# Performance work log

Hardware: AMD Instinct MI355X
Metric: run time of the kernel (lower is better)

Reference implementation:

```python
import jax, jax.numpy as jnp
import numpy as np

N, E, IN, HID, OUT, H, G = 50000, 800000, 128, 32, 32, 4, 64
NEG_SLOPE = 0.2


def setup_inputs() -> dict:
    key = jax.random.key(0)
    ks = jax.random.split(key, 12)
    p = lambda k, s: jax.random.normal(k, s, jnp.float32) * 0.1
    x = jax.random.normal(ks[0], (N, IN), jnp.float32)
    edge_index = jax.random.randint(ks[1], (2, E), 0, N, dtype=jnp.int64)
    batch = jnp.sort(jax.random.randint(ks[2], (N,), 0, G, dtype=jnp.int64))
    return {
        'x': x, 'edge_index': edge_index, 'batch': batch,
        'W1': p(ks[3], (IN, H * HID)),
        'att_src1': p(ks[4], (H, HID)), 'att_dst1': p(ks[5], (H, HID)),
        'b1': jnp.zeros((H * HID,), jnp.float32),
        'W2': p(ks[6], (H * HID, H * OUT)),
        'att_src2': p(ks[7], (H, OUT)), 'att_dst2': p(ks[8], (H, OUT)),
        'b2': jnp.zeros((H * OUT,), jnp.float32),
        'lin_w': p(ks[9], (H * OUT, 1)),
        'lin_b': jnp.zeros((1,), jnp.float32),
    }


def gat_conv(x, src, dst, W, a_src, a_dst, b, heads, ch):
    # x: [N, F_in]; src/dst: [E'] with self-loops already appended.
    n = x.shape[0]
    h = (x @ W).reshape(n, heads, ch)                      # [N, H, C]
    alpha_s = jnp.einsum('nhc,hc->nh', h, a_src)           # [N, H]
    alpha_d = jnp.einsum('nhc,hc->nh', h, a_dst)
    e = jax.nn.leaky_relu(alpha_s[src] + alpha_d[dst], NEG_SLOPE)  # [E', H]
    # segment softmax over destination neighborhoods
    m = jax.ops.segment_max(e, dst, num_segments=n)
    m = jnp.where(jnp.isfinite(m), m, 0.0)
    ex = jnp.exp(e - m[dst])
    s = jax.ops.segment_sum(ex, dst, num_segments=n)
    alpha = ex / (s[dst] + 1e-16)                          # [E', H]
    out = jax.ops.segment_sum(alpha[:, :, None] * h[src], dst, num_segments=n)
    return out.reshape(n, heads * ch) + b


def reference(x, edge_index, batch, W1, att_src1, att_dst1, b1,
              W2, att_src2, att_dst2, b2, lin_w, lin_b):
    # add self-loops (PyG GATConv default add_self_loops=True)
    loops = jnp.arange(N, dtype=edge_index.dtype)
    src = jnp.concatenate([edge_index[0], loops])
    dst = jnp.concatenate([edge_index[1], loops])

    h = jax.nn.elu(gat_conv(x, src, dst, W1, att_src1, att_dst1, b1, H, HID))
    h = gat_conv(h, src, dst, W2, att_src2, att_dst2, b2, H, OUT)  # [N, H*OUT]

    # global mean + max pool per graph
    counts = jax.ops.segment_sum(jnp.ones((N,), h.dtype), batch, num_segments=G)
    mean_p = jax.ops.segment_sum(h, batch, num_segments=G) / jnp.maximum(counts, 1.0)[:, None]
    max_p = jax.ops.segment_max(h, batch, num_segments=G)
    max_p = jnp.where(jnp.isfinite(max_p), max_p, 0.0)
    pooled = mean_p + max_p                                # [G, H*OUT]
    return pooled @ lin_w + lin_b                          # [G, 1]
```

## Files before the change

kernel.cpp:

```cpp
#include <hip/hip_runtime.h>
#include <hip/hip_bf16.h>
#include <hip/hip_fp16.h>
#include <math.h>

#define NEG_SLOPE 0.2f
#define BCAP 64
#define LAYER_W 18432

typedef _Float16 half8 __attribute__((ext_vector_type(8)));
typedef _Float16 half4v __attribute__((ext_vector_type(4)));
typedef float f32x4 __attribute__((ext_vector_type(4)));


__device__ __forceinline__ int lbound(const int* __restrict__ a, int n, int key) {
    int lo = 0, hi = n;
    while (lo < hi) {
        int mid = (lo + hi) >> 1;
        if (a[mid] < key) lo = mid + 1; else hi = mid;
    }
    return lo;
}

__device__ __forceinline__ unsigned encf(float f) {
    unsigned u = __float_as_uint(f);
    return (u & 0x80000000u) ? ~u : (u | 0x80000000u);
}
__device__ __forceinline__ float decf(unsigned u) {
    return (u & 0x80000000u) ? __uint_as_float(u & 0x7FFFFFFFu) : __uint_as_float(~u);
}


__global__ void prep_kernel(const float* __restrict__ W1, const float* __restrict__ W2,
                            const float* __restrict__ as1, const float* __restrict__ ad1,
                            const float* __restrict__ as2, const float* __restrict__ ad2,
                            _Float16* __restrict__ wt_hi, _Float16* __restrict__ wt_lo,
                            int* __restrict__ cnt, float* __restrict__ gsum,
                            unsigned* __restrict__ gmax, unsigned short* __restrict__ col,
                            int n, int gtot) {
    int b = blockIdx.x;
    if (b < 72) {
        int lane = threadIdx.x;
        if (lane >= 64) return;
        int layer = b / 36;
        int rem = b % 36;
        int nt = rem >> 2;
        int kc = rem & 3;
        const float* W  = layer ? W2 : W1;
        const float* As = layer ? as2 : as1;
        const float* Ad = layer ? ad2 : ad1;
        int nn = lane & 15, q = lane >> 4;
        size_t base = (size_t)layer * LAYER_W + (size_t)((nt * 4 + kc) * 64 + lane) * 8;
        #pragma unroll
        for (int j = 0; j < 8; ++j) {
            int k = kc * 32 + q * 8 + j;
            float w = 0.f;
            if (nt < 8) {
                w = W[(size_t)k * 128 + nt * 16 + nn];
            } else if (nn < 4) {
                for (int c = 0; c < 32; ++c) w += W[(size_t)k * 128 + nn * 32 + c] * As[nn * 32 + c];
            } else if (nn < 8) {
                int hh = nn - 4;
                for (int c = 0; c < 32; ++c) w += W[(size_t)k * 128 + hh * 32 + c] * Ad[hh * 32 + c];
            }
            _Float16 hi = (_Float16)w;
            wt_hi[base + j] = hi;
            wt_lo[base + j] = (_Float16)(w - (float)hi);
        }
        return;
    }
    int i = (b - 72) * 256 + threadIdx.x;
    if (i < n) cnt[i] = 0;
    if (i < gtot) { gsum[i] = 0.f; gmax[i] = 0u; }
    if (i < n * 8) ((uint4*)col)[i] = make_uint4(0u, 0u, 0u, 0u);
}


__global__ void build_kernel(const int* __restrict__ src, const int* __restrict__ dst,
                             int* __restrict__ cnt, unsigned short* __restrict__ col,
                             int E, int n) {
    int part = blockIdx.x & 7;
    int bb   = blockIdx.x >> 3;
    int nb   = gridDim.x >> 3;
    int psz  = (n + 7) >> 3;
    int lo   = part * psz;
    int total = E + n;
    for (int i = bb * 256 + threadIdx.x; i < total; i += nb * 256) {
        int d = (i < E) ? dst[i] : (i - E);
        if (d < lo || d >= lo + psz) continue;
        int slot = atomicAdd(&cnt[d], 1);
        if (slot < BCAP) {
            int s = (i < E) ? src[i] : d;
            col[(size_t)d * BCAP + slot] = (unsigned short)s;
        }
    }
}


template <bool A16>
__global__ __launch_bounds__(256) void gemm_attn_kernel(
        const void* __restrict__ Araw,
        const _Float16* __restrict__ wt_hi, const _Float16* __restrict__ wt_lo,
        _Float16* __restrict__ H16, float* __restrict__ as_, float* __restrict__ ad_,
        int M) {
    __shared__ _Float16 a_st[128][136];

    int tid = threadIdx.x;
    int m0 = blockIdx.x * 128;

    if (A16) {
        const _Float16* A = (const _Float16*)Araw;
        #pragma unroll
        for (int t = 0; t < 8; ++t) {
            int f = tid + t * 256;
            int r = f >> 4;
            int c8 = (f & 15) << 3;
            int gr = m0 + r; if (gr >= M) gr = M - 1;
            *(half8*)&a_st[r][c8] = *(const half8*)(A + (size_t)gr * 128 + c8);
        }
    } else {
        const float* A = (const float*)Araw;
        #pragma unroll
        for (int t = 0; t < 16; ++t) {
            int f = tid + t * 256;
            int r = f >> 5;
            int c4 = (f & 31) << 2;
            int gr = m0 + r; if (gr >= M) gr = M - 1;
            const float4 v = *(const float4*)(A + (size_t)gr * 128 + c4);
            half4v hi = { (_Float16)v.x, (_Float16)v.y, (_Float16)v.z, (_Float16)v.w };
            *(half4v*)&a_st[r][c4] = hi;
        }
    }
    __syncthreads();

    int w = tid >> 6;
    int lane = tid & 63;
    int cbase = lane & 15;
    int q = lane >> 4;
    int mrow0 = (w << 5) + cbase;
    int mrow1 = mrow0 + 16;

    f32x4 acc0[9], acc1[9];
    #pragma unroll
    for (int nt = 0; nt < 9; ++nt) {
        acc0[nt] = (f32x4){0.f, 0.f, 0.f, 0.f};
        acc1[nt] = (f32x4){0.f, 0.f, 0.f, 0.f};
    }

    #pragma unroll
    for (int kc = 0; kc < 4; ++kc) {
        half8 ah0 = *(half8*)&a_st[mrow0][kc * 32 + q * 8];
        half8 ah1 = *(half8*)&a_st[mrow1][kc * 32 + q * 8];
        #pragma unroll
        for (int nt = 0; nt < 9; ++nt) {
            const half8 bh = *(const half8*)(wt_hi + (size_t)((nt * 4 + kc) * 64 + lane) * 8);
            const half8 bl = *(const half8*)(wt_lo + (size_t)((nt * 4 + kc) * 64 + lane) * 8);
            acc0[nt] = __builtin_amdgcn_mfma_f32_16x16x32_f16(ah0, bh, acc0[nt], 0, 0, 0);
            acc0[nt] = __builtin_amdgcn_mfma_f32_16x16x32_f16(ah0, bl, acc0[nt], 0, 0, 0);
            acc1[nt] = __builtin_amdgcn_mfma_f32_16x16x32_f16(ah1, bh, acc1[nt], 0, 0, 0);
            acc1[nt] = __builtin_amdgcn_mfma_f32_16x16x32_f16(ah1, bl, acc1[nt], 0, 0, 0);
        }
    }

    #pragma unroll
    for (int nt = 0; nt < 8; ++nt) {
        int c = nt * 16 + cbase;
        #pragma unroll
        for (int i = 0; i < 4; ++i) {
            int gr0 = m0 + (w << 5) + (q << 2) + i;
            int gr1 = gr0 + 16;
            if (gr0 < M) H16[(size_t)gr0 * 128 + c] = (_Float16)acc0[nt][i];
            if (gr1 < M) H16[(size_t)gr1 * 128 + c] = (_Float16)acc1[nt][i];
        }
    }
    if (cbase < 8) {
        #pragma unroll
        for (int i = 0; i < 4; ++i) {
            int gr0 = m0 + (w << 5) + (q << 2) + i;
            int gr1 = gr0 + 16;
            if (gr0 < M) {
                if (cbase < 4) as_[(size_t)gr0 * 4 + cbase]     = acc0[8][i];
                else           ad_[(size_t)gr0 * 4 + cbase - 4] = acc0[8][i];
            }
            if (gr1 < M) {
                if (cbase < 4) as_[(size_t)gr1 * 4 + cbase]     = acc1[8][i];
                else           ad_[(size_t)gr1 * 4 + cbase - 4] = acc1[8][i];
            }
        }
    }
}


__global__ __launch_bounds__(256) void agg_kernel(
        const int* __restrict__ cnt, const unsigned short* __restrict__ col,
        const _Float16* __restrict__ h16, const float* __restrict__ as_,
        const float* __restrict__ ad_, const float* __restrict__ bias,
        _Float16* __restrict__ out16, int n, int elu) {
    __shared__ float s_w[4][4][64];

    int wvb  = threadIdx.x >> 6;
    int lane = threadIdx.x & 63;
    int wv   = blockIdx.x * 4 + wvb;
    int valid = (wv < n);
    if (!valid) wv = n - 1;

    const unsigned short* crow = col + (size_t)wv * BCAP;
    int q = lane >> 4;
    int r = lane & 15;
    int head = r >> 2;
    unsigned roff = (unsigned)r << 4;
    const char* hbyte = (const char*)h16;

    ushort4 cr0 = *(const ushort4*)(crow + 4 * q);
    ushort4 cr1 = *(const ushort4*)(crow + 16 + 4 * q);
    half8 ha0 = *(const half8*)(hbyte + (((unsigned)cr0.x << 8) | roff));
    half8 ha1 = *(const half8*)(hbyte + (((unsigned)cr0.y << 8) | roff));
    half8 ha2 = *(const half8*)(hbyte + (((unsigned)cr0.z << 8) | roff));
    half8 ha3 = *(const half8*)(hbyte + (((unsigned)cr0.w << 8) | roff));
    half8 hb0 = *(const half8*)(hbyte + (((unsigned)cr1.x << 8) | roff));
    half8 hb1 = *(const half8*)(hbyte + (((unsigned)cr1.y << 8) | roff));
    half8 hb2 = *(const half8*)(hbyte + (((unsigned)cr1.z << 8) | roff));
    half8 hb3 = *(const half8*)(hbyte + (((unsigned)cr1.w << 8) | roff));

    int deg = cnt[wv]; if (deg > BCAP) deg = BCAP;

    const float4 adv = *(const float4*)(ad_ + (size_t)wv * 4);
    float w0 = 0.f, w1 = 0.f, w2 = 0.f, w3 = 0.f;
    if (lane < deg) {
        int s = crow[lane];
        const float4 av = *(const float4*)(as_ + (size_t)s * 4);
        float e0 = av.x + adv.x, e1 = av.y + adv.y;
        float e2 = av.z + adv.z, e3 = av.w + adv.w;
        w0 = __expf(fmaxf(e0, NEG_SLOPE * e0));
        w1 = __expf(fmaxf(e1, NEG_SLOPE * e1));
        w2 = __expf(fmaxf(e2, NEG_SLOPE * e2));
        w3 = __expf(fmaxf(e3, NEG_SLOPE * e3));
    }
    s_w[wvb][0][lane] = w0;
    s_w[wvb][1][lane] = w1;
    s_w[wvb][2][lane] = w2;
    s_w[wvb][3][lane] = w3;
    asm volatile("s_waitcnt lgkmcnt(0)" ::: "memory");

    f32x4 wa = *(const f32x4*)&s_w[wvb][head][4 * q];
    f32x4 wb = *(const f32x4*)&s_w[wvb][head][16 + 4 * q];
    float lsum = (wa.x + wa.y + wa.z + wa.w) + (wb.x + wb.y + wb.z + wb.w);
    float acc[8];
    #pragma unroll
    for (int j = 0; j < 8; ++j)
        acc[j] = wa.x * (float)ha0[j] + wa.y * (float)ha1[j]
               + wa.z * (float)ha2[j] + wa.w * (float)ha3[j]
               + wb.x * (float)hb0[j] + wb.y * (float)hb1[j]
               + wb.z * (float)hb2[j] + wb.w * (float)hb3[j];

    if (__builtin_expect(deg > 32, 0)) {
        for (int base = 32; base < deg; base += 16) {
            ushort4 cr = *(const ushort4*)(crow + base + 4 * q);
            half8 t0 = *(const half8*)(hbyte + (((unsigned)cr.x << 8) | roff));
            half8 t1 = *(const half8*)(hbyte + (((unsigned)cr.y << 8) | roff));
            half8 t2 = *(const half8*)(hbyte + (((unsigned)cr.z << 8) | roff));
            half8 t3 = *(const half8*)(hbyte + (((unsigned)cr.w << 8) | roff));
            f32x4 wt = *(const f32x4*)&s_w[wvb][head][base + 4 * q];
            lsum += wt.x + wt.y + wt.z + wt.w;
            #pragma unroll
            for (int j = 0; j < 8; ++j)
                acc[j] += wt.x * (float)t0[j] + wt.y * (float)t1[j]
                        + wt.z * (float)t2[j] + wt.w * (float)t3[j];
        }
    }

    #pragma unroll
    for (int j = 0; j < 8; ++j) {
        acc[j] += __shfl_xor(acc[j], 16, 64);
        acc[j] += __shfl_xor(acc[j], 32, 64);
    }
    lsum += __shfl_xor(lsum, 16, 64);
    lsum += __shfl_xor(lsum, 32, 64);

    if (lane < 16 && valid) {
        float inv = 1.f / (lsum + 1e-16f);
        const float4 bv0 = *(const float4*)(bias + 8 * r);
        const float4 bv1 = *(const float4*)(bias + 8 * r + 4);
        float o[8];
        o[0] = acc[0] * inv + bv0.x; o[1] = acc[1] * inv + bv0.y;
        o[2] = acc[2] * inv + bv0.z; o[3] = acc[3] * inv + bv0.w;
        o[4] = acc[4] * inv + bv1.x; o[5] = acc[5] * inv + bv1.y;
        o[6] = acc[6] * inv + bv1.z; o[7] = acc[7] * inv + bv1.w;
        if (elu) {
            #pragma unroll
            for (int j = 0; j < 8; ++j) o[j] = o[j] > 0.f ? o[j] : expm1f(o[j]);
        }
        half8 hv;
        #pragma unroll
        for (int j = 0; j < 8; ++j) hv[j] = (_Float16)o[j];
        *(half8*)(out16 + (size_t)wv * 128 + 8 * r) = hv;
    }
}


__global__ void pool1_kernel(const _Float16* __restrict__ h, const int* __restrict__ batch,
                             float* __restrict__ gsum, unsigned* __restrict__ gmax, int n) {
    int g = blockIdx.x >> 3;
    int p = blockIdx.x & 7;
    int c = threadIdx.x;
    int s = lbound(batch, n, g);
    int e = lbound(batch, n, g + 1);
    int len = e - s;
    int lo = s + (int)((long long)len * p / 8);
    int hi = s + (int)((long long)len * (p + 1) / 8);
    float sum = 0.f, mx = -INFINITY;
    for (int i = lo; i < hi; ++i) {
        float v = (float)h[(size_t)i * 128 + c];
        sum += v; mx = fmaxf(mx, v);
    }
    if (hi > lo) {
        atomicAdd(&gsum[g * 128 + c], sum);
        atomicMax(&gmax[g * 128 + c], encf(mx));
    }
}

__global__ void pool2_kernel(const float* __restrict__ gsum, const unsigned* __restrict__ gmax,
                             const int* __restrict__ batch, const float* __restrict__ lin_w,
                             const float* __restrict__ lin_b, float* __restrict__ out, int n) {
    int g = blockIdx.x;
    int c = threadIdx.x;
    int s = lbound(batch, n, g);
    int e = lbound(batch, n, g + 1);
    float cnt = fmaxf((float)(e - s), 1.0f);
    float mean = gsum[g * 128 + c] / cnt;
    float mx = decf(gmax[g * 128 + c]);
    if (!isfinite(mx)) mx = 0.f;
    float v = (mean + mx) * lin_w[c];
    __shared__ float red[128];
    red[c] = v;
    __syncthreads();
    for (int off = 64; off > 0; off >>= 1) {
        if (c < off) red[c] += red[c + off];
        __syncthreads();
    }
    if (c == 0) out[g] = red[0] + lin_b[0];
}


extern "C" void kernel_launch(void* const* d_in, const int* in_sizes, int n_in,
                              void* d_out, int out_size, void* d_ws, size_t ws_size,
                              hipStream_t stream) {
    const float* x    = (const float*)d_in[0];
    const int*   ei   = (const int*)d_in[1];
    const int*   batch= (const int*)d_in[2];
    const float* W1   = (const float*)d_in[3];
    const float* at_s1= (const float*)d_in[4];
    const float* at_d1= (const float*)d_in[5];
    const float* b1   = (const float*)d_in[6];
    const float* W2   = (const float*)d_in[7];
    const float* at_s2= (const float*)d_in[8];
    const float* at_d2= (const float*)d_in[9];
    const float* b2   = (const float*)d_in[10];
    const float* lw   = (const float*)d_in[11];
    const float* lb   = (const float*)d_in[12];
    float* out = (float*)d_out;

    const int N = in_sizes[0] / 128;
    const int E = in_sizes[1] / 2;
    const int G = out_size;

    char* p = (char*)d_ws;
    auto carve = [&](size_t bytes) -> void* {
        void* q = (void*)p;
        p += (bytes + 255) & ~(size_t)255;
        return q;
    };
    _Float16*       h16   = (_Float16*)carve((size_t)N * 128 * 2);
    _Float16*       a16   = (_Float16*)carve((size_t)N * 128 * 2);
    _Float16*       p16   = (_Float16*)carve((size_t)N * 128 * 2);
    float*          asb   = (float*)carve((size_t)N * 4 * 4);
    float*          adb   = (float*)carve((size_t)N * 4 * 4);
    int*            cnt   = (int*)carve((size_t)N * 4);
    unsigned short* col   = (unsigned short*)carve((size_t)N * BCAP * 2);
    float*          gsum  = (float*)carve((size_t)G * 128 * 4);
    unsigned*       gmax  = (unsigned*)carve((size_t)G * 128 * 4);
    _Float16*       wt_hi = (_Float16*)carve((size_t)2 * LAYER_W * 2);
    _Float16*       wt_lo = (_Float16*)carve((size_t)2 * LAYER_W * 2);

    const int* esrc = ei;
    const int* edst = ei + E;

    int initN = N * 8;
    if (initN < G * 128) initN = G * 128;
    prep_kernel<<<72 + (initN + 255) / 256, 256, 0, stream>>>(
        W1, W2, at_s1, at_d1, at_s2, at_d2, wt_hi, wt_lo, cnt, gsum, gmax, col, N, G * 128);

    build_kernel<<<512 * 8, 256, 0, stream>>>(esrc, edst, cnt, col, E, N);

    gemm_attn_kernel<false><<<(N + 127) / 128, 256, 0, stream>>>(
        x, wt_hi, wt_lo, h16, asb, adb, N);
    agg_kernel<<<(N + 3) / 4, 256, 0, stream>>>(
        cnt, col, h16, asb, adb, b1, a16, N, 1);

    gemm_attn_kernel<true><<<(N + 127) / 128, 256, 0, stream>>>(
        a16, wt_hi + LAYER_W, wt_lo + LAYER_W, h16, asb, adb, N);
    agg_kernel<<<(N + 3) / 4, 256, 0, stream>>>(
        cnt, col, h16, asb, adb, b2, p16, N, 0);

    pool1_kernel<<<G * 8, 128, 0, stream>>>(p16, batch, gsum, gmax, N);
    pool2_kernel<<<G, 128, 0, stream>>>(gsum, gmax, batch, lw, lb, out, N);
}
```

Before: 285.8 us.

## Fuse second-layer aggregation with global pooling and shrink GEMM tiles

Fuses the layer-2 aggregation with the mean/max pooling. Each node atomically updates the per-graph max and adds its dot product with lin_w to a per-graph scalar, so the p16 intermediate and the pool1 pass are no longer needed. The mean term is folded algebraically into the linear head. Separately, the GEMM block is halved to 64 rows and 128 threads for more blocks and occupancy. The cost is heavy atomic contention on the gmax entries, since 64 graphs each receive about 128 atomics from every node.

```diff
diff --git a/kernel.cpp b/kernel.cpp
--- a/kernel.cpp
+++ b/kernel.cpp
@@ -34,7 +34,7 @@
                             const float* __restrict__ as1, const float* __restrict__ ad1,
                             const float* __restrict__ as2, const float* __restrict__ ad2,
                             _Float16* __restrict__ wt_hi, _Float16* __restrict__ wt_lo,
-                            int* __restrict__ cnt, float* __restrict__ gsum,
+                            int* __restrict__ cnt, float* __restrict__ gsumDot,
                             unsigned* __restrict__ gmax, unsigned short* __restrict__ col,
                             int n, int gtot) {
     int b = blockIdx.x;
@@ -70,7 +70,8 @@
     }
     int i = (b - 72) * 256 + threadIdx.x;
     if (i < n) cnt[i] = 0;
-    if (i < gtot) { gsum[i] = 0.f; gmax[i] = 0u; }
+    if (i < gtot) gmax[i] = 0u;
+    if (i < gtot / 128) gsumDot[i] = 0.f;
     if (i < n * 8) ((uint4*)col)[i] = make_uint4(0u, 0u, 0u, 0u);
 }
 
@@ -97,21 +98,21 @@
 
 
 template <bool A16>
-__global__ __launch_bounds__(256) void gemm_attn_kernel(
+__global__ __launch_bounds__(128) void gemm_attn_kernel(
         const void* __restrict__ Araw,
         const _Float16* __restrict__ wt_hi, const _Float16* __restrict__ wt_lo,
         _Float16* __restrict__ H16, float* __restrict__ as_, float* __restrict__ ad_,
         int M) {
-    __shared__ _Float16 a_st[128][136];
+    __shared__ _Float16 a_st[64][136];
 
     int tid = threadIdx.x;
-    int m0 = blockIdx.x * 128;
+    int m0 = blockIdx.x * 64;
 
     if (A16) {
         const _Float16* A = (const _Float16*)Araw;
         #pragma unroll
         for (int t = 0; t < 8; ++t) {
-            int f = tid + t * 256;
+            int f = tid + t * 128;
             int r = f >> 4;
             int c8 = (f & 15) << 3;
             int gr = m0 + r; if (gr >= M) gr = M - 1;
@@ -121,7 +122,7 @@
         const float* A = (const float*)Araw;
         #pragma unroll
         for (int t = 0; t < 16; ++t) {
-            int f = tid + t * 256;
+            int f = tid + t * 128;
             int r = f >> 5;
             int c4 = (f & 31) << 2;
             int gr = m0 + r; if (gr >= M) gr = M - 1;
@@ -194,7 +195,7 @@
         const int* __restrict__ cnt, const unsigned short* __restrict__ col,
         const _Float16* __restrict__ h16, const float* __restrict__ as_,
         const float* __restrict__ ad_, const float* __restrict__ bias,
-        _Float16* __restrict__ out16, int n, int elu) {
+        _Float16* __restrict__ out16, int n) {
     __shared__ float s_w[4][4][64];
 
     int wvb  = threadIdx.x >> 6;
@@ -285,10 +286,8 @@
         o[2] = acc[2] * inv + bv0.z; o[3] = acc[3] * inv + bv0.w;
         o[4] = acc[4] * inv + bv1.x; o[5] = acc[5] * inv + bv1.y;
         o[6] = acc[6] * inv + bv1.z; o[7] = acc[7] * inv + bv1.w;
-        if (elu) {
-            #pragma unroll
-            for (int j = 0; j < 8; ++j) o[j] = o[j] > 0.f ? o[j] : expm1f(o[j]);
-        }
+        #pragma unroll
+        for (int j = 0; j < 8; ++j) o[j] = o[j] > 0.f ? o[j] : expm1f(o[j]);
         half8 hv;
         #pragma unroll
         for (int j = 0; j < 8; ++j) hv[j] = (_Float16)o[j];
@@ -297,39 +296,131 @@
 }
 
 
-__global__ void pool1_kernel(const _Float16* __restrict__ h, const int* __restrict__ batch,
-                             float* __restrict__ gsum, unsigned* __restrict__ gmax, int n) {
-    int g = blockIdx.x >> 3;
-    int p = blockIdx.x & 7;
-    int c = threadIdx.x;
-    int s = lbound(batch, n, g);
-    int e = lbound(batch, n, g + 1);
-    int len = e - s;
-    int lo = s + (int)((long long)len * p / 8);
-    int hi = s + (int)((long long)len * (p + 1) / 8);
-    float sum = 0.f, mx = -INFINITY;
-    for (int i = lo; i < hi; ++i) {
-        float v = (float)h[(size_t)i * 128 + c];
-        sum += v; mx = fmaxf(mx, v);
-    }
-    if (hi > lo) {
-        atomicAdd(&gsum[g * 128 + c], sum);
-        atomicMax(&gmax[g * 128 + c], encf(mx));
-    }
-}
-
-__global__ void pool2_kernel(const float* __restrict__ gsum, const unsigned* __restrict__ gmax,
-                             const int* __restrict__ batch, const float* __restrict__ lin_w,
-                             const float* __restrict__ lin_b, float* __restrict__ out, int n) {
+__global__ __launch_bounds__(256) void agg_pool_kernel(
+        const int* __restrict__ cnt, const unsigned short* __restrict__ col,
+        const _Float16* __restrict__ h16, const float* __restrict__ as_,
+        const float* __restrict__ ad_, const float* __restrict__ bias,
+        const int* __restrict__ batch, const float* __restrict__ lin_w,
+        float* __restrict__ gsumDot, unsigned* __restrict__ gmax, int n) {
+    __shared__ float s_w[4][4][64];
+
+    int wvb  = threadIdx.x >> 6;
+    int lane = threadIdx.x & 63;
+    int wv   = blockIdx.x * 4 + wvb;
+    int valid = (wv < n);
+    if (!valid) wv = n - 1;
+
+    const unsigned short* crow = col + (size_t)wv * BCAP;
+    int q = lane >> 4;
+    int r = lane & 15;
+    int head = r >> 2;
+    unsigned roff = (unsigned)r << 4;
+    const char* hbyte = (const char*)h16;
+
+    ushort4 cr0 = *(const ushort4*)(crow + 4 * q);
+    ushort4 cr1 = *(const ushort4*)(crow + 16 + 4 * q);
+    half8 ha0 = *(const half8*)(hbyte + (((unsigned)cr0.x << 8) | roff));
+    half8 ha1 = *(const half8*)(hbyte + (((unsigned)cr0.y << 8) | roff));
+    half8 ha2 = *(const half8*)(hbyte + (((unsigned)cr0.z << 8) | roff));
+    half8 ha3 = *(const half8*)(hbyte + (((unsigned)cr0.w << 8) | roff));
+    half8 hb0 = *(const half8*)(hbyte + (((unsigned)cr1.x << 8) | roff));
+    half8 hb1 = *(const half8*)(hbyte + (((unsigned)cr1.y << 8) | roff));
+    half8 hb2 = *(const half8*)(hbyte + (((unsigned)cr1.z << 8) | roff));
+    half8 hb3 = *(const half8*)(hbyte + (((unsigned)cr1.w << 8) | roff));
+
+    int deg = cnt[wv]; if (deg > BCAP) deg = BCAP;
+
+    const float4 adv = *(const float4*)(ad_ + (size_t)wv * 4);
+    float w0 = 0.f, w1 = 0.f, w2 = 0.f, w3 = 0.f;
+    if (lane < deg) {
+        int s = crow[lane];
+        const float4 av = *(const float4*)(as_ + (size_t)s * 4);
+        float e0 = av.x + adv.x, e1 = av.y + adv.y;
+        float e2 = av.z + adv.z, e3 = av.w + adv.w;
+        w0 = __expf(fmaxf(e0, NEG_SLOPE * e0));
+        w1 = __expf(fmaxf(e1, NEG_SLOPE * e1));
+        w2 = __expf(fmaxf(e2, NEG_SLOPE * e2));
+        w3 = __expf(fmaxf(e3, NEG_SLOPE * e3));
+    }
+    s_w[wvb][0][lane] = w0;
+    s_w[wvb][1][lane] = w1;
+    s_w[wvb][2][lane] = w2;
+    s_w[wvb][3][lane] = w3;
+    asm volatile("s_waitcnt lgkmcnt(0)" ::: "memory");
+
+    f32x4 wa = *(const f32x4*)&s_w[wvb][head][4 * q];
+    f32x4 wb = *(const f32x4*)&s_w[wvb][head][16 + 4 * q];
+    float lsum = (wa.x + wa.y + wa.z + wa.w) + (wb.x + wb.y + wb.z + wb.w);
+    float acc[8];
+    #pragma unroll
+    for (int j = 0; j < 8; ++j)
+        acc[j] = wa.x * (float)ha0[j] + wa.y * (float)ha1[j]
+               + wa.z * (float)ha2[j] + wa.w * (float)ha3[j]
+               + wb.x * (float)hb0[j] + wb.y * (float)hb1[j]
+               + wb.z * (float)hb2[j] + wb.w * (float)hb3[j];
+
+    if (__builtin_expect(deg > 32, 0)) {
+        for (int base = 32; base < deg; base += 16) {
+            ushort4 cr = *(const ushort4*)(crow + base + 4 * q);
+            half8 t0 = *(const half8*)(hbyte + (((unsigned)cr.x << 8) | roff));
+            half8 t1 = *(const half8*)(hbyte + (((unsigned)cr.y << 8) | roff));
+            half8 t2 = *(const half8*)(hbyte + (((unsigned)cr.z << 8) | roff));
+            half8 t3 = *(const half8*)(hbyte + (((unsigned)cr.w << 8) | roff));
+            f32x4 wt = *(const f32x4*)&s_w[wvb][head][base + 4 * q];
+            lsum += wt.x + wt.y + wt.z + wt.w;
+            #pragma unroll
+            for (int j = 0; j < 8; ++j)
+                acc[j] += wt.x * (float)t0[j] + wt.y * (float)t1[j]
+                        + wt.z * (float)t2[j] + wt.w * (float)t3[j];
+        }
+    }
+
+    #pragma unroll
+    for (int j = 0; j < 8; ++j) {
+        acc[j] += __shfl_xor(acc[j], 16, 64);
+        acc[j] += __shfl_xor(acc[j], 32, 64);
+    }
+    lsum += __shfl_xor(lsum, 16, 64);
+    lsum += __shfl_xor(lsum, 32, 64);
+
+    if (lane < 16 && valid) {
+        float inv = 1.f / (lsum + 1e-16f);
+        const float4 bv0 = *(const float4*)(bias + 8 * r);
+        const float4 bv1 = *(const float4*)(bias + 8 * r + 4);
+        float o[8];
+        o[0] = acc[0] * inv + bv0.x; o[1] = acc[1] * inv + bv0.y;
+        o[2] = acc[2] * inv + bv0.z; o[3] = acc[3] * inv + bv0.w;
+        o[4] = acc[4] * inv + bv1.x; o[5] = acc[5] * inv + bv1.y;
+        o[6] = acc[6] * inv + bv1.z; o[7] = acc[7] * inv + bv1.w;
+
+        int g = batch[wv];
+        unsigned* gm = gmax + (size_t)g * 128 + 8 * r;
+        #pragma unroll
+        for (int j = 0; j < 8; ++j) atomicMax(&gm[j], encf(o[j]));
+        const float4 lw0 = *(const float4*)(lin_w + 8 * r);
+        const float4 lw1 = *(const float4*)(lin_w + 8 * r + 4);
+        float dot = o[0] * lw0.x + o[1] * lw0.y + o[2] * lw0.z + o[3] * lw0.w
+                  + o[4] * lw1.x + o[5] * lw1.y + o[6] * lw1.z + o[7] * lw1.w;
+        dot += __shfl_xor(dot, 1, 64);
+        dot += __shfl_xor(dot, 2, 64);
+        dot += __shfl_xor(dot, 4, 64);
+        dot += __shfl_xor(dot, 8, 64);
+        if (r == 0) atomicAdd(&gsumDot[g], dot);
+    }
+}
+
+
+__global__ void pool_final_kernel(const float* __restrict__ gsumDot,
+                                  const unsigned* __restrict__ gmax,
+                                  const int* __restrict__ batch,
+                                  const float* __restrict__ lin_w,
+                                  const float* __restrict__ lin_b,
+                                  float* __restrict__ out, int n) {
     int g = blockIdx.x;
     int c = threadIdx.x;
-    int s = lbound(batch, n, g);
-    int e = lbound(batch, n, g + 1);
-    float cnt = fmaxf((float)(e - s), 1.0f);
-    float mean = gsum[g * 128 + c] / cnt;
     float mx = decf(gmax[g * 128 + c]);
     if (!isfinite(mx)) mx = 0.f;
-    float v = (mean + mx) * lin_w[c];
+    float v = mx * lin_w[c];
     __shared__ float red[128];
     red[c] = v;
     __syncthreads();
@@ -337,7 +428,12 @@
         if (c < off) red[c] += red[c + off];
         __syncthreads();
     }
-    if (c == 0) out[g] = red[0] + lin_b[0];
+    if (c == 0) {
+        int s = lbound(batch, n, g);
+        int e = lbound(batch, n, g + 1);
+        float cnt = fmaxf((float)(e - s), 1.0f);
+        out[g] = red[0] + gsumDot[g] / cnt + lin_b[0];
+    }
 }
 
 
@@ -371,12 +467,11 @@
     };
     _Float16*       h16   = (_Float16*)carve((size_t)N * 128 * 2);
     _Float16*       a16   = (_Float16*)carve((size_t)N * 128 * 2);
-    _Float16*       p16   = (_Float16*)carve((size_t)N * 128 * 2);
     float*          asb   = (float*)carve((size_t)N * 4 * 4);
     float*          adb   = (float*)carve((size_t)N * 4 * 4);
     int*            cnt   = (int*)carve((size_t)N * 4);
     unsigned short* col   = (unsigned short*)carve((size_t)N * BCAP * 2);
-    float*          gsum  = (float*)carve((size_t)G * 128 * 4);
+    float*          gsumDot = (float*)carve((size_t)G * 4);
     unsigned*       gmax  = (unsigned*)carve((size_t)G * 128 * 4);
     _Float16*       wt_hi = (_Float16*)carve((size_t)2 * LAYER_W * 2);
     _Float16*       wt_lo = (_Float16*)carve((size_t)2 * LAYER_W * 2);
@@ -387,20 +482,19 @@
     int initN = N * 8;
     if (initN < G * 128) initN = G * 128;
     prep_kernel<<<72 + (initN + 255) / 256, 256, 0, stream>>>(
-        W1, W2, at_s1, at_d1, at_s2, at_d2, wt_hi, wt_lo, cnt, gsum, gmax, col, N, G * 128);
+        W1, W2, at_s1, at_d1, at_s2, at_d2, wt_hi, wt_lo, cnt, gsumDot, gmax, col, N, G * 128);
 
     build_kernel<<<512 * 8, 256, 0, stream>>>(esrc, edst, cnt, col, E, N);
 
-    gemm_attn_kernel<false><<<(N + 127) / 128, 256, 0, stream>>>(
+    gemm_attn_kernel<false><<<(N + 63) / 64, 128, 0, stream>>>(
         x, wt_hi, wt_lo, h16, asb, adb, N);
     agg_kernel<<<(N + 3) / 4, 256, 0, stream>>>(
-        cnt, col, h16, asb, adb, b1, a16, N, 1);
-
-    gemm_attn_kernel<true><<<(N + 127) / 128, 256, 0, stream>>>(
+        cnt, col, h16, asb, adb, b1, a16, N);
+
+    gemm_attn_kernel<true><<<(N + 63) / 64, 128, 0, stream>>>(
         a16, wt_hi + LAYER_W, wt_lo + LAYER_W, h16, asb, adb, N);
-    agg_kernel<<<(N + 3) / 4, 256, 0, stream>>>(
-        cnt, col, h16, asb, adb, b2, p16, N, 0);
-
-    pool1_kernel<<<G * 8, 128, 0, stream>>>(p16, batch, gsum, gmax, N);
-    pool2_kernel<<<G, 128, 0, stream>>>(gsum, gmax, batch, lw, lb, out, N);
-}
+    agg_pool_kernel<<<(N + 3) / 4, 256, 0, stream>>>(
+        cnt, col, h16, asb, adb, b2, batch, lw, gsumDot, gmax, N);
+
+    pool_final_kernel<<<G, 128, 0, stream>>>(gsumDot, gmax, batch, lw, lb, out, N);
+}
```

New measurement: 710.2 us. 149% more time.
